# Optimization experiments

Measured on AMD Instinct MI355X. Metric: run time of the kernel, lower is better.

## Reference

```python
import jax, jax.numpy as jnp
import numpy as np
import math

IN_CH = 256; ORDER = 8; K = 9; B = 32; L = 8192


def _conv1d(x, w, b, dilation, padding):
    # x: [B,C,L], w: [O,C,k]
    y = jax.lax.conv_general_dilated(x, w, (1,), [(padding, padding)],
                                     rhs_dilation=(dilation,),
                                     dimension_numbers=('NCH', 'OIH', 'NCH'))
    return y + b[None, :, None]


def _bn(x, g, beta, eps=1e-5):
    # training-mode BatchNorm1d: batch statistics over (B, L), biased variance
    m = x.mean(axis=(0, 2), keepdims=True)
    v = ((x - m) ** 2).mean(axis=(0, 2), keepdims=True)
    return g[None, :, None] * (x - m) * jax.lax.rsqrt(v + eps) + beta[None, :, None]


def _adaptive_r(x, p):
    # p = (c1w,c1b,c2w,c2b,g1,b1,g2,b2,g3,b3,pxw,pxb,fcw,fcb)
    a = jax.nn.relu(_bn(_conv1d(x, p[0], p[1], 1, 1), p[4], p[5]))
    b2 = jax.nn.relu(_bn(_conv1d(x, p[2], p[3], 2, 2), p[6], p[7]))
    c = jax.nn.relu(_bn(_conv1d(a + b2, p[10], p[11], 1, 0), p[8], p[9]))
    pooled = c.mean(axis=2)                      # AdaptiveAvgPool1d(1) + flatten
    return pooled @ p[12].T + p[13]              # [B,1]


def _hermite_kernel(t):
    # t: [B,K] -> kernel [B, ORDER, K]
    hs = [jnp.ones_like(t), 2.0 * t]
    for i in range(2, ORDER - 1):
        hs.append(2.0 * t * hs[-1] - 2.0 * (i - 1) * hs[-2])
    exp_term = jnp.exp(-0.5 * t * t)
    fs = []
    for i in range(ORDER - 1):
        const = 2.0 ** (i / 2) / math.sqrt(math.pi * math.factorial(i))
        f = exp_term * (const * hs[i])
        norm = jnp.linalg.norm(f, axis=1, keepdims=True)
        fs.append(f / jnp.clip(norm, 1e-12))
    fs.append(jax.nn.sigmoid(2.0 * t))           # 1/(1+exp(-2t))
    return jnp.stack(fs, axis=1)


def _forward(x, conv1_w, conv1_b, conv2_b, wp, cp):
    # conv1 is kernel-size-1 -> pointwise GEMM
    x1 = jnp.einsum('bil,oi->bol', x, conv1_w[:, :, 0]) + conv1_b[None, :, None]
    width = _adaptive_r(x1, wp)                  # [B,1]
    center = jnp.clip(_adaptive_r(x1, cp), 1.0, 128.0)
    T = jnp.arange(K, dtype=x.dtype)[None, :]
    t = width * (T - center)                     # [B,K]
    kernel = _hermite_kernel(t)                  # [B,ORDER,K]
    # batched per-sample conv1d (the torch loop over B) as one einsum pass
    pad = K // 2
    Lx = x1.shape[2]
    x1p = jnp.pad(x1, ((0, 0), (0, 0), (pad, pad)))
    out = sum(jnp.einsum('bcl,bc->bl', x1p[:, :, j:j + Lx], kernel[:, :, j])
              for j in range(K))
    out = out[:, None, :] + conv2_b[None, :, None]   # [B,1,L]
    return out, x1


def setup_inputs() -> dict:
    key = jax.random.key(0)
    ks = iter(jax.random.split(key, 64))
    def rn(shape, s=0.05):
        return jax.random.normal(next(ks), shape, dtype=jnp.float32) * s
    d = {
        'x': jax.random.normal(next(ks), (B, IN_CH, L), dtype=jnp.float32),
        'conv1_w': rn((ORDER, IN_CH, 1)),
        'conv1_b': jnp.zeros((ORDER,), jnp.float32),
        'conv2_b': jnp.zeros((1,), jnp.float32),
    }
    for pre in ('w_', 'c_'):
        d[pre + 'c1w'] = rn((ORDER, ORDER, 3)); d[pre + 'c1b'] = jnp.zeros((ORDER,), jnp.float32)
        d[pre + 'c2w'] = rn((ORDER, ORDER, 3)); d[pre + 'c2b'] = jnp.zeros((ORDER,), jnp.float32)
        for g in ('g1', 'g2', 'g3'):
            d[pre + g] = jnp.ones((ORDER,), jnp.float32)
        for bn in ('b1', 'b2', 'b3'):
            d[pre + bn] = jnp.zeros((ORDER,), jnp.float32)
        d[pre + 'pxw'] = rn((ORDER, ORDER, 1)); d[pre + 'pxb'] = jnp.zeros((ORDER,), jnp.float32)
        d[pre + 'fcw'] = rn((1, ORDER), 0.1); d[pre + 'fcb'] = jnp.zeros((1,), jnp.float32)
    return d


def reference(x, conv1_w, conv1_b, conv2_b,
              w_c1w, w_c1b, w_c2w, w_c2b, w_g1, w_b1, w_g2, w_b2, w_g3, w_b3,
              w_pxw, w_pxb, w_fcw, w_fcb,
              c_c1w, c_c1b, c_c2w, c_c2b, c_g1, c_b1, c_g2, c_b2, c_g3, c_b3,
              c_pxw, c_pxb, c_fcw, c_fcb):
    wp = (w_c1w, w_c1b, w_c2w, w_c2b, w_g1, w_b1, w_g2, w_b2, w_g3, w_b3,
          w_pxw, w_pxb, w_fcw, w_fcb)
    cp = (c_c1w, c_c1b, c_c2w, c_c2b, c_g1, c_b1, c_g2, c_b2, c_g3, c_b3,
          c_pxw, c_pxb, c_fcw, c_fcb)
    return _forward(x, conv1_w, conv1_b, conv2_b, wp, cp)
```

## Files before the change

### kernel.cpp

```cpp
#include <hip/hip_runtime.h>
#include <math.h>

#define BATCH 32
#define CIN   256
#define LEN   8192
#define HL    (LEN/2)
#define ORD   8
#define NPOS  (BATCH*LEN)

struct Params { const float* p[32]; };



__device__ __forceinline__ void load_conv_lds(const Params& P, float* wl, float* bl, int tid)
{
    for (int idx = tid; idx < 4*192; idx += 256) {
        int which = idx / 192, s = idx - which*192;
        const float* src = (which==0) ? P.p[4] : (which==1) ? P.p[6]
                         : (which==2) ? P.p[18] : P.p[20];
        wl[idx] = src[s];
    }
    if (tid < 32) {
        int wq = tid >> 3, o = tid & 7;
        const float* bsrc = (wq==0) ? P.p[5] : (wq==1) ? P.p[7]
                          : (wq==2) ? P.p[19] : P.p[21];
        bl[tid] = bsrc[o];
    }
}

__device__ __forceinline__ float conv6(
    const float xv[8][6], const float* wl, const float* bl, int bc, int o, int s)
{
    float a = bl[bc*8 + o];
    const float* wr = &wl[(bc*8 + o)*24];
    if ((bc & 1) == 0) {
#pragma unroll
        for (int i = 0; i < 8; i++)
            a += wr[i*3+0]*xv[i][s+1] + wr[i*3+1]*xv[i][s+2] + wr[i*3+2]*xv[i][s+3];
    } else {
#pragma unroll
        for (int i = 0; i < 8; i++)
            a += wr[i*3+0]*xv[i][s+0] + wr[i*3+1]*xv[i][s+2] + wr[i*3+2]*xv[i][s+4];
    }
    return a;
}

__device__ __forceinline__ void wave_reduce2(float& sv, float& sq)
{
#pragma unroll
    for (int m = 32; m >= 1; m >>= 1) {
        sv += __shfl_xor(sv, m, 64);
        sq += __shfl_xor(sq, m, 64);
    }
}
__device__ __forceinline__ void wave_reduce1(float& sv)
{
#pragma unroll
    for (int m = 32; m >= 1; m >>= 1) sv += __shfl_xor(sv, m, 64);
}

#define XT_W 520
#define LOAD_XV6(xt, tid, xv)                                 \
    _Pragma("unroll")                                         \
    for (int i_ = 0; i_ < 8; i_++) {                          \
        _Pragma("unroll")                                     \
        for (int d_ = 0; d_ < 6; d_++)                        \
            xv[i_][d_] = xt[i_][2 + 2*(tid) + d_];            \
    }

__device__ __forceinline__ void stage_tile(
    const float* __restrict__ x1, int b, int t0, float (*xt)[XT_W], int tid)
{
    int ch = tid >> 5, q = tid & 31;
    const float* src = x1 + ((size_t)b*ORD + ch)*LEN + t0 + q*16;
    float4* dst = reinterpret_cast<float4*>(&xt[ch][4 + q*16]);
#pragma unroll
    for (int j = 0; j < 4; j++) dst[j] = reinterpret_cast<const float4*>(src)[j];
    if (tid < 32) {
        int hc = tid >> 2, hh = tid & 3;
        int l   = t0 + ((hh < 2) ? (hh - 2) : (510 + hh));
        int idx = (hh < 2) ? (2 + hh) : (514 + hh);
        xt[hc][idx] = ((unsigned)l < (unsigned)LEN)
                    ? x1[((size_t)b*ORD + hc)*LEN + l] : 0.f;
    }
}

__global__ __launch_bounds__(256, 2) void k1_gemm_stats(
    const float* __restrict__ x, const float* __restrict__ w,
    const float* __restrict__ bias, float* __restrict__ x1,
    float* __restrict__ ws, Params P)
{
    __shared__ float wt[CIN][ORD];
    __shared__ float wl[768], bl[32];
    __shared__ float xt[8][XT_W];
    __shared__ float part[256];
    int tid = threadIdx.x;
    for (int idx = tid; idx < CIN*ORD; idx += 256) {
        int o = idx >> 8, i = idx & 255;
        wt[i][o] = w[idx];
    }
    load_conv_lds(P, wl, bl, tid);
    __syncthreads();

    int b  = blockIdx.x >> 4;
    int t0 = (blockIdx.x & 15) << 9;

    const float2* xrow = reinterpret_cast<const float2*>(x)
                       + (size_t)b*CIN*HL + (t0 >> 1) + tid;
    float2 acc[ORD];
#pragma unroll
    for (int o = 0; o < ORD; o++) { acc[o].x = 0.f; acc[o].y = 0.f; }

#pragma unroll 8
    for (int i = 0; i < CIN; i++) {
        float2 xv2 = xrow[(size_t)i * HL];
        const float4* wr = reinterpret_cast<const float4*>(&wt[i][0]);
        float4 wa = wr[0], wb = wr[1];
        acc[0].x += xv2.x*wa.x; acc[0].y += xv2.y*wa.x;
        acc[1].x += xv2.x*wa.y; acc[1].y += xv2.y*wa.y;
        acc[2].x += xv2.x*wa.z; acc[2].y += xv2.y*wa.z;
        acc[3].x += xv2.x*wa.w; acc[3].y += xv2.y*wa.w;
        acc[4].x += xv2.x*wb.x; acc[4].y += xv2.y*wb.x;
        acc[5].x += xv2.x*wb.y; acc[5].y += xv2.y*wb.y;
        acc[6].x += xv2.x*wb.z; acc[6].y += xv2.y*wb.z;
        acc[7].x += xv2.x*wb.w; acc[7].y += xv2.y*wb.w;
    }

    float2* x1row = reinterpret_cast<float2*>(x1)
                  + (size_t)b*ORD*HL + (t0 >> 1) + tid;
#pragma unroll
    for (int o = 0; o < ORD; o++) {
        float bo = bias[o];
        float2 r; r.x = acc[o].x + bo; r.y = acc[o].y + bo;
        x1row[(size_t)o * HL] = r;
        *reinterpret_cast<float2*>(&xt[o][4 + 2*tid]) = r;
    }

    if (tid < 32) {
        int hp = tid >> 3, ch = tid & 7;
        int l  = t0 + ((hp < 2) ? (hp - 2) : (510 + hp));
        float a = 0.f;
        if ((unsigned)l < (unsigned)LEN) {
            const float* xp = x + (size_t)b*CIN*LEN + l;
#pragma unroll 4
            for (int i = 0; i < CIN; i++) a += xp[(size_t)i*LEN] * wt[i][ch];
            a += bias[ch];
        }
        int idx = (hp < 2) ? (2 + hp) : (514 + hp);
        xt[ch][idx] = a;
    }
    __syncthreads();

    float xv[8][6];
    LOAD_XV6(xt, tid, xv);

    int lane = tid & 63, wv = tid >> 6;
#pragma unroll
    for (int bc = 0; bc < 4; bc++) {
#pragma unroll
        for (int o = 0; o < 8; o++) {
            float a0 = conv6(xv, wl, bl, bc, o, 0);
            float a1 = conv6(xv, wl, bl, bc, o, 1);
            float sv = a0 + a1, sq = a0*a0 + a1*a1;
            wave_reduce2(sv, sq);
            if (lane == 0) {
                int c = bc*8 + o;
                part[c*4 + wv] = sv; part[(32+c)*4 + wv] = sq;
            }
        }
    }
    __syncthreads();
    if (tid < 64) {
        float s = part[tid*4] + part[tid*4+1] + part[tid*4+2] + part[tid*4+3];
        atomicAdd(&ws[tid], s);
    }
}

__global__ __launch_bounds__(256, 2) void k3_cpre_stats(
    const float* __restrict__ x1, float* __restrict__ ws, Params P)
{
    __shared__ float wl[768], bl[32];
    __shared__ float pxl[128], pxbl[16];
    __shared__ float scl[32], shf[32];
    __shared__ float xt[8][XT_W];
    __shared__ float part[128];
    int tid = threadIdx.x;
    load_conv_lds(P, wl, bl, tid);
    if (tid < 128) pxl[tid]  = (tid < 64) ? P.p[14][tid] : P.p[28][tid-64];
    if (tid < 16)  pxbl[tid] = (tid < 8)  ? P.p[15][tid] : P.p[29][tid-8];
    if (tid >= 128 && tid < 160) {
        int c = tid - 128;
        int br = c >> 4, cv = (c >> 3) & 1, o = c & 7;
        const float Ninv = 1.0f / (float)NPOS;
        float m   = ws[c]      * Ninv;
        float var = ws[32 + c] * Ninv - m*m;
        const float* g  = P.p[ br ? (cv?23:22) : (cv?9:8)  ];
        const float* be = P.p[ br ? (cv?26:25) : (cv?12:11)];
        float sc = g[o] * rsqrtf(var + 1e-5f);
        scl[c] = sc; shf[c] = be[o] - m*sc;
    }
    int b  = blockIdx.x >> 4;
    int t0 = (blockIdx.x & 15) << 9;
    stage_tile(x1, b, t0, xt, tid);
    __syncthreads();

    float xv[8][6];
    LOAD_XV6(xt, tid, xv);

    int lane = tid & 63, wv = tid >> 6;
#pragma unroll
    for (int br = 0; br < 2; br++) {
        float s0[8], s1[8];
#pragma unroll
        for (int ch = 0; ch < 8; ch++) {
            int ca = (br*2+0)*8 + ch, cb = (br*2+1)*8 + ch;
            s0[ch] = fmaxf(conv6(xv,wl,bl,br*2+0,ch,0)*scl[ca] + shf[ca], 0.f)
                   + fmaxf(conv6(xv,wl,bl,br*2+1,ch,0)*scl[cb] + shf[cb], 0.f);
            s1[ch] = fmaxf(conv6(xv,wl,bl,br*2+0,ch,1)*scl[ca] + shf[ca], 0.f)
                   + fmaxf(conv6(xv,wl,bl,br*2+1,ch,1)*scl[cb] + shf[cb], 0.f);
        }
#pragma unroll
        for (int o = 0; o < 8; o++) {
            float a0 = pxbl[br*8 + o], a1 = a0;
#pragma unroll
            for (int i = 0; i < 8; i++) {
                a0 += pxl[br*64 + o*8 + i] * s0[i];
                a1 += pxl[br*64 + o*8 + i] * s1[i];
            }
            float sv = a0 + a1, sq = a0*a0 + a1*a1;
            wave_reduce2(sv, sq);
            if (lane == 0) {
                int c = br*8 + o;
                part[c*4 + wv] = sv; part[(16+c)*4 + wv] = sq;
            }
        }
    }
    __syncthreads();
    if (tid < 32) {
        float s = part[tid*4] + part[tid*4+1] + part[tid*4+2] + part[tid*4+3];
        atomicAdd(&ws[64 + tid], s);
    }
}

__global__ __launch_bounds__(256, 2) void k4_csum(
    const float* __restrict__ x1, float* __restrict__ ws, Params P)
{
    __shared__ float wl[768], bl[32];
    __shared__ float pxl[128], pxbl[16];
    __shared__ float scl[32], shf[32];
    __shared__ float scl3[16], shf3[16];
    __shared__ float xt[8][XT_W];
    __shared__ float part[64];
    int tid = threadIdx.x;
    load_conv_lds(P, wl, bl, tid);
    if (tid < 128) pxl[tid]  = (tid < 64) ? P.p[14][tid] : P.p[28][tid-64];
    if (tid < 16)  pxbl[tid] = (tid < 8)  ? P.p[15][tid] : P.p[29][tid-8];
    const float Ninv = 1.0f / (float)NPOS;
    if (tid >= 128 && tid < 160) {
        int c = tid - 128;
        int br = c >> 4, cv = (c >> 3) & 1, o = c & 7;
        float m   = ws[c]      * Ninv;
        float var = ws[32 + c] * Ninv - m*m;
        const float* g  = P.p[ br ? (cv?23:22) : (cv?9:8)  ];
        const float* be = P.p[ br ? (cv?26:25) : (cv?12:11)];
        float sc = g[o] * rsqrtf(var + 1e-5f);
        scl[c] = sc; shf[c] = be[o] - m*sc;
    }
    if (tid >= 160 && tid < 176) {
        int c = tid - 160;
        int br = c >> 3, o = c & 7;
        float m3 = ws[64 + c] * Ninv;
        float v3 = ws[80 + c] * Ninv - m3*m3;
        const float* g3 = P.p[ br ? 24 : 10 ];
        const float* b3 = P.p[ br ? 27 : 13 ];
        float sc = g3[o] * rsqrtf(v3 + 1e-5f);
        scl3[c] = sc; shf3[c] = b3[o] - m3*sc;
    }
    int b  = blockIdx.x >> 4;
    int t0 = (blockIdx.x & 15) << 9;
    stage_tile(x1, b, t0, xt, tid);
    __syncthreads();

    float xv[8][6];
    LOAD_XV6(xt, tid, xv);

    int lane = tid & 63, wv = tid >> 6;
#pragma unroll
    for (int br = 0; br < 2; br++) {
        float s0[8], s1[8];
#pragma unroll
        for (int ch = 0; ch < 8; ch++) {
            int ca = (br*2+0)*8 + ch, cb = (br*2+1)*8 + ch;
            s0[ch] = fmaxf(conv6(xv,wl,bl,br*2+0,ch,0)*scl[ca] + shf[ca], 0.f)
                   + fmaxf(conv6(xv,wl,bl,br*2+1,ch,0)*scl[cb] + shf[cb], 0.f);
            s1[ch] = fmaxf(conv6(xv,wl,bl,br*2+0,ch,1)*scl[ca] + shf[ca], 0.f)
                   + fmaxf(conv6(xv,wl,bl,br*2+1,ch,1)*scl[cb] + shf[cb], 0.f);
        }
#pragma unroll
        for (int o = 0; o < 8; o++) {
            float a0 = pxbl[br*8 + o], a1 = a0;
#pragma unroll
            for (int i = 0; i < 8; i++) {
                a0 += pxl[br*64 + o*8 + i] * s0[i];
                a1 += pxl[br*64 + o*8 + i] * s1[i];
            }
            int c = br*8 + o;
            float v0 = fmaxf(a0*scl3[c] + shf3[c], 0.f);
            float v1 = fmaxf(a1*scl3[c] + shf3[c], 0.f);
            float sv = v0 + v1;
            wave_reduce1(sv);
            if (lane == 0) part[c*4 + wv] = sv;
        }
    }
    __syncthreads();
    if (tid < 16) {
        float s = part[tid*4] + part[tid*4+1] + part[tid*4+2] + part[tid*4+3];
        atomicAdd(&ws[96 + (tid >> 3)*256 + b*8 + (tid & 7)], s);
    }
}

#define XT6_W 272
__global__ __launch_bounds__(256) void k6_out(
    const float* __restrict__ x1, const float* __restrict__ ws, Params P,
    float* __restrict__ out)
{
    __shared__ float kern[8][9];
    __shared__ float xt[8][XT6_W];
    int tid = threadIdx.x;
    int b  = blockIdx.x >> 5;
    int t0 = (blockIdx.x & 31) << 8;

    {
        int ch = tid >> 5, q = tid & 31;
        const float* src = x1 + ((size_t)b*ORD + ch)*LEN + t0;
        float4 a0 = *reinterpret_cast<const float4*>(src + q*8);
        float4 a1 = *reinterpret_cast<const float4*>(src + q*8 + 4);
        *reinterpret_cast<float4*>(&xt[ch][8  + q*8]) = a0;
        *reinterpret_cast<float4*>(&xt[ch][12 + q*8]) = a1;
        if (q < 4) {
            int l = t0 - 4 + q;
            xt[ch][4 + q] = (l >= 0) ? src[q - 4] : 0.f;
        } else if (q < 8) {
            int l = t0 + 256 + (q - 4);
            xt[ch][260 + q] = (l < LEN) ? src[256 + q - 4] : 0.f;
        }
    }

    if (tid < 9) {
        const float Li = 1.0f / (float)LEN;
        float vw = P.p[17][0], vc = P.p[31][0];
#pragma unroll
        for (int ch = 0; ch < 8; ch++) {
            vw += P.p[16][ch] * (ws[96 +       b*8 + ch] * Li);
            vc += P.p[30][ch] * (ws[96 + 256 + b*8 + ch] * Li);
        }
        float width  = vw;
        float center = fminf(fmaxf(vc, 1.0f), 128.0f);

        float cst[7];
        cst[0] = 0.56418958354775628f;
#pragma unroll
        for (int i = 1; i < 7; i++) cst[i] = cst[i-1] * sqrtf(2.0f / (float)i);

        int k = tid;
        float t = width * ((float)k - center);
        float e = expf(-0.5f * t * t);
        float hp = 1.0f, hc = 2.0f * t;
        kern[0][k] = e * cst[0];
        kern[1][k] = e * cst[1] * hc;
#pragma unroll
        for (int i = 2; i < 7; i++) {
            float hn = 2.0f*t*hc - 2.0f*(float)(i-1)*hp;
            hp = hc; hc = hn;
            kern[i][k] = e * cst[i] * hc;
        }
        kern[7][k] = 1.0f / (1.0f + expf(-2.0f * t));
    }
    __syncthreads();
    if (tid < 7) {
        float ss = 0.f;
#pragma unroll
        for (int k = 0; k < 9; k++) ss += kern[tid][k]*kern[tid][k];
        float inv = 1.0f / fmaxf(sqrtf(ss), 1e-12f);
#pragma unroll
        for (int k = 0; k < 9; k++) kern[tid][k] *= inv;
    }
    __syncthreads();

    float acc = P.p[3][0];
#pragma unroll
    for (int c = 0; c < 8; c++) {
#pragma unroll
        for (int j = 0; j < 9; j++) acc += xt[c][4 + tid + j] * kern[c][j];
    }
    out[(size_t)b*LEN + t0 + tid] = acc;
}

extern "C" void kernel_launch(void* const* d_in, const int* in_sizes, int n_in,
                              void* d_out, int out_size, void* d_ws, size_t ws_size,
                              hipStream_t stream)
{
    (void)in_sizes; (void)n_in; (void)out_size; (void)ws_size;
    const float* x  = (const float*)d_in[0];
    const float* w1 = (const float*)d_in[1];
    const float* b1 = (const float*)d_in[2];
    float* outF = (float*)d_out;
    float* x1   = outF + (size_t)BATCH * LEN;
    float* ws   = (float*)d_ws;

    Params P;
    for (int i = 0; i < 32; i++) P.p[i] = (const float*)d_in[i];

    hipMemsetAsync(d_ws, 0, 4096, stream);
    k1_gemm_stats<<<512,  256, 0, stream>>>(x, w1, b1, x1, ws, P);
    k3_cpre_stats<<<512,  256, 0, stream>>>(x1, ws, P);
    k4_csum      <<<512,  256, 0, stream>>>(x1, ws, P);
    k6_out       <<<1024, 256, 0, stream>>>(x1, ws, P, outF);
}
```

Baseline: 142.6 us.

## Materialize pre-BN3 activations to skip recomputing convs in csum pass

The third stats pass no longer recomputes the dilated convolutions and pointwise mix. It now reads 16 pre-BN channels that the second pass writes to workspace, which trades compute for an extra write and read of about 32 MB. The GEMM kernel also loads its halo inputs with a coalesced per-channel load into LDS instead of strided global reads. Conv weights are now read directly through restrict pointers rather than staged in LDS. The workspace must be large enough to hold cpre.

```diff
diff --git a/kernel.cpp b/kernel.cpp
--- a/kernel.cpp
+++ b/kernel.cpp
@@ -12,37 +12,24 @@
 
 
 
-__device__ __forceinline__ void load_conv_lds(const Params& P, float* wl, float* bl, int tid)
-{
-    for (int idx = tid; idx < 4*192; idx += 256) {
-        int which = idx / 192, s = idx - which*192;
-        const float* src = (which==0) ? P.p[4] : (which==1) ? P.p[6]
-                         : (which==2) ? P.p[18] : P.p[20];
-        wl[idx] = src[s];
-    }
-    if (tid < 32) {
-        int wq = tid >> 3, o = tid & 7;
-        const float* bsrc = (wq==0) ? P.p[5] : (wq==1) ? P.p[7]
-                          : (wq==2) ? P.p[19] : P.p[21];
-        bl[tid] = bsrc[o];
-    }
-}
-
-__device__ __forceinline__ float conv6(
-    const float xv[8][6], const float* wl, const float* bl, int bc, int o, int s)
-{
-    float a = bl[bc*8 + o];
-    const float* wr = &wl[(bc*8 + o)*24];
-    if ((bc & 1) == 0) {
-#pragma unroll
-        for (int i = 0; i < 8; i++)
-            a += wr[i*3+0]*xv[i][s+1] + wr[i*3+1]*xv[i][s+2] + wr[i*3+2]*xv[i][s+3];
-    } else {
-#pragma unroll
-        for (int i = 0; i < 8; i++)
-            a += wr[i*3+0]*xv[i][s+0] + wr[i*3+1]*xv[i][s+2] + wr[i*3+2]*xv[i][s+4];
-    }
-    return a;
+__device__ __forceinline__ void conv6_pair(
+    const float xv[8][6], const float* __restrict__ w, float bv, int dil, int o,
+    float& r0, float& r1)
+{
+    float a0 = bv, a1 = bv;
+    const float* wr = w + o*24;
+#pragma unroll
+    for (int i = 0; i < 8; i++) {
+        float w0 = wr[i*3+0], w1 = wr[i*3+1], w2 = wr[i*3+2];
+        if (dil == 1) {
+            a0 += w0*xv[i][1] + w1*xv[i][2] + w2*xv[i][3];
+            a1 += w0*xv[i][2] + w1*xv[i][3] + w2*xv[i][4];
+        } else {
+            a0 += w0*xv[i][0] + w1*xv[i][2] + w2*xv[i][4];
+            a1 += w0*xv[i][1] + w1*xv[i][3] + w2*xv[i][5];
+        }
+    }
+    r0 = a0; r1 = a1;
 }
 
 __device__ __forceinline__ void wave_reduce2(float& sv, float& sq)
@@ -88,22 +75,30 @@
 __global__ __launch_bounds__(256, 2) void k1_gemm_stats(
     const float* __restrict__ x, const float* __restrict__ w,
     const float* __restrict__ bias, float* __restrict__ x1,
-    float* __restrict__ ws, Params P)
+    float* __restrict__ ws,
+    const float* __restrict__ wA, const float* __restrict__ bA,
+    const float* __restrict__ wB, const float* __restrict__ bB,
+    const float* __restrict__ wC, const float* __restrict__ bC,
+    const float* __restrict__ wD, const float* __restrict__ bD)
 {
     __shared__ float wt[CIN][ORD];
-    __shared__ float wl[768], bl[32];
     __shared__ float xt[8][XT_W];
+    __shared__ float hbuf[4][257];
     __shared__ float part[256];
     int tid = threadIdx.x;
     for (int idx = tid; idx < CIN*ORD; idx += 256) {
         int o = idx >> 8, i = idx & 255;
         wt[i][o] = w[idx];
     }
-    load_conv_lds(P, wl, bl, tid);
-    __syncthreads();
 
     int b  = blockIdx.x >> 4;
     int t0 = (blockIdx.x & 15) << 9;
+
+    const float* xch = x + ((size_t)b*CIN + tid)*LEN;
+    float h0 = 0.f, h1 = 0.f, h2 = 0.f, h3 = 0.f;
+    if (t0 >= 2)        { h0 = xch[t0-2];   h1 = xch[t0-1]; }
+    if (t0 + 513 < LEN) { h2 = xch[t0+512]; h3 = xch[t0+513]; }
+    __syncthreads();
 
     const float2* xrow = reinterpret_cast<const float2*>(x)
                        + (size_t)b*CIN*HL + (t0 >> 1) + tid;
@@ -135,16 +130,17 @@
         x1row[(size_t)o * HL] = r;
         *reinterpret_cast<float2*>(&xt[o][4 + 2*tid]) = r;
     }
+    hbuf[0][tid] = h0; hbuf[1][tid] = h1; hbuf[2][tid] = h2; hbuf[3][tid] = h3;
+    __syncthreads();
 
     if (tid < 32) {
         int hp = tid >> 3, ch = tid & 7;
         int l  = t0 + ((hp < 2) ? (hp - 2) : (510 + hp));
         float a = 0.f;
         if ((unsigned)l < (unsigned)LEN) {
-            const float* xp = x + (size_t)b*CIN*LEN + l;
-#pragma unroll 4
-            for (int i = 0; i < CIN; i++) a += xp[(size_t)i*LEN] * wt[i][ch];
-            a += bias[ch];
+            a = bias[ch];
+#pragma unroll 8
+            for (int i = 0; i < CIN; i++) a += hbuf[hp][i] * wt[i][ch];
         }
         int idx = (hp < 2) ? (2 + hp) : (514 + hp);
         xt[ch][idx] = a;
@@ -156,15 +152,18 @@
 
     int lane = tid & 63, wv = tid >> 6;
 #pragma unroll
-    for (int bc = 0; bc < 4; bc++) {
+    for (int grp = 0; grp < 4; grp++) {
+        const float* wg = (grp==0) ? wA : (grp==1) ? wB : (grp==2) ? wC : wD;
+        const float* bg = (grp==0) ? bA : (grp==1) ? bB : (grp==2) ? bC : bD;
+        int dil = (grp & 1) ? 2 : 1;
 #pragma unroll
         for (int o = 0; o < 8; o++) {
-            float a0 = conv6(xv, wl, bl, bc, o, 0);
-            float a1 = conv6(xv, wl, bl, bc, o, 1);
+            float a0, a1;
+            conv6_pair(xv, wg, bg[o], dil, o, a0, a1);
             float sv = a0 + a1, sq = a0*a0 + a1*a1;
             wave_reduce2(sv, sq);
             if (lane == 0) {
-                int c = bc*8 + o;
+                int c = grp*8 + o;
                 part[c*4 + wv] = sv; part[(32+c)*4 + wv] = sq;
             }
         }
@@ -177,17 +176,19 @@
 }
 
 __global__ __launch_bounds__(256, 2) void k3_cpre_stats(
-    const float* __restrict__ x1, float* __restrict__ ws, Params P)
-{
-    __shared__ float wl[768], bl[32];
-    __shared__ float pxl[128], pxbl[16];
+    const float* __restrict__ x1,
+    const float* __restrict__ wA, const float* __restrict__ bA,
+    const float* __restrict__ wB, const float* __restrict__ bB,
+    const float* __restrict__ wC, const float* __restrict__ bC,
+    const float* __restrict__ wD, const float* __restrict__ bD,
+    const float* __restrict__ pxA, const float* __restrict__ pxbA,
+    const float* __restrict__ pxB, const float* __restrict__ pxbB,
+    float* __restrict__ ws, float* __restrict__ cpre, Params P)
+{
     __shared__ float scl[32], shf[32];
     __shared__ float xt[8][XT_W];
     __shared__ float part[128];
     int tid = threadIdx.x;
-    load_conv_lds(P, wl, bl, tid);
-    if (tid < 128) pxl[tid]  = (tid < 64) ? P.p[14][tid] : P.p[28][tid-64];
-    if (tid < 16)  pxbl[tid] = (tid < 8)  ? P.p[15][tid] : P.p[29][tid-8];
     if (tid >= 128 && tid < 160) {
         int c = tid - 128;
         int br = c >> 4, cv = (c >> 3) & 1, o = c & 7;
@@ -210,27 +211,37 @@
     int lane = tid & 63, wv = tid >> 6;
 #pragma unroll
     for (int br = 0; br < 2; br++) {
+        const float* w1p = br ? wC : wA;  const float* b1p = br ? bC : bA;
+        const float* w2p = br ? wD : wB;  const float* b2p = br ? bD : bB;
+        const float* pxp = br ? pxB : pxA;
+        const float* pbp = br ? pxbB : pxbA;
         float s0[8], s1[8];
 #pragma unroll
         for (int ch = 0; ch < 8; ch++) {
             int ca = (br*2+0)*8 + ch, cb = (br*2+1)*8 + ch;
-            s0[ch] = fmaxf(conv6(xv,wl,bl,br*2+0,ch,0)*scl[ca] + shf[ca], 0.f)
-                   + fmaxf(conv6(xv,wl,bl,br*2+1,ch,0)*scl[cb] + shf[cb], 0.f);
-            s1[ch] = fmaxf(conv6(xv,wl,bl,br*2+0,ch,1)*scl[ca] + shf[ca], 0.f)
-                   + fmaxf(conv6(xv,wl,bl,br*2+1,ch,1)*scl[cb] + shf[cb], 0.f);
+            float a0, a1, c0, c1;
+            conv6_pair(xv, w1p, b1p[ch], 1, ch, a0, a1);
+            conv6_pair(xv, w2p, b2p[ch], 2, ch, c0, c1);
+            s0[ch] = fmaxf(a0*scl[ca] + shf[ca], 0.f)
+                   + fmaxf(c0*scl[cb] + shf[cb], 0.f);
+            s1[ch] = fmaxf(a1*scl[ca] + shf[ca], 0.f)
+                   + fmaxf(c1*scl[cb] + shf[cb], 0.f);
         }
 #pragma unroll
         for (int o = 0; o < 8; o++) {
-            float a0 = pxbl[br*8 + o], a1 = a0;
+            float a0 = pbp[o], a1 = a0;
 #pragma unroll
             for (int i = 0; i < 8; i++) {
-                a0 += pxl[br*64 + o*8 + i] * s0[i];
-                a1 += pxl[br*64 + o*8 + i] * s1[i];
+                a0 += pxp[o*8 + i] * s0[i];
+                a1 += pxp[o*8 + i] * s1[i];
             }
+            int c = br*8 + o;
+            float2 st; st.x = a0; st.y = a1;
+            *reinterpret_cast<float2*>(
+                &cpre[(size_t)c*NPOS + (size_t)b*LEN + t0 + 2*tid]) = st;
             float sv = a0 + a1, sq = a0*a0 + a1*a1;
             wave_reduce2(sv, sq);
             if (lane == 0) {
-                int c = br*8 + o;
                 part[c*4 + wv] = sv; part[(16+c)*4 + wv] = sq;
             }
         }
@@ -242,75 +253,35 @@
     }
 }
 
-__global__ __launch_bounds__(256, 2) void k4_csum(
-    const float* __restrict__ x1, float* __restrict__ ws, Params P)
-{
-    __shared__ float wl[768], bl[32];
-    __shared__ float pxl[128], pxbl[16];
-    __shared__ float scl[32], shf[32];
+__global__ __launch_bounds__(256) void k4_light(
+    const float* __restrict__ cpre, float* __restrict__ ws, Params P)
+{
     __shared__ float scl3[16], shf3[16];
-    __shared__ float xt[8][XT_W];
     __shared__ float part[64];
     int tid = threadIdx.x;
-    load_conv_lds(P, wl, bl, tid);
-    if (tid < 128) pxl[tid]  = (tid < 64) ? P.p[14][tid] : P.p[28][tid-64];
-    if (tid < 16)  pxbl[tid] = (tid < 8)  ? P.p[15][tid] : P.p[29][tid-8];
     const float Ninv = 1.0f / (float)NPOS;
-    if (tid >= 128 && tid < 160) {
-        int c = tid - 128;
-        int br = c >> 4, cv = (c >> 3) & 1, o = c & 7;
-        float m   = ws[c]      * Ninv;
-        float var = ws[32 + c] * Ninv - m*m;
-        const float* g  = P.p[ br ? (cv?23:22) : (cv?9:8)  ];
-        const float* be = P.p[ br ? (cv?26:25) : (cv?12:11)];
-        float sc = g[o] * rsqrtf(var + 1e-5f);
-        scl[c] = sc; shf[c] = be[o] - m*sc;
-    }
-    if (tid >= 160 && tid < 176) {
-        int c = tid - 160;
-        int br = c >> 3, o = c & 7;
-        float m3 = ws[64 + c] * Ninv;
-        float v3 = ws[80 + c] * Ninv - m3*m3;
+    if (tid < 16) {
+        int br = tid >> 3, o = tid & 7;
+        float m3 = ws[64 + tid] * Ninv;
+        float v3 = ws[80 + tid] * Ninv - m3*m3;
         const float* g3 = P.p[ br ? 24 : 10 ];
         const float* b3 = P.p[ br ? 27 : 13 ];
         float sc = g3[o] * rsqrtf(v3 + 1e-5f);
-        scl3[c] = sc; shf3[c] = b3[o] - m3*sc;
-    }
+        scl3[tid] = sc; shf3[tid] = b3[o] - m3*sc;
+    }
+    __syncthreads();
+
     int b  = blockIdx.x >> 4;
     int t0 = (blockIdx.x & 15) << 9;
-    stage_tile(x1, b, t0, xt, tid);
-    __syncthreads();
-
-    float xv[8][6];
-    LOAD_XV6(xt, tid, xv);
-
     int lane = tid & 63, wv = tid >> 6;
 #pragma unroll
-    for (int br = 0; br < 2; br++) {
-        float s0[8], s1[8];
-#pragma unroll
-        for (int ch = 0; ch < 8; ch++) {
-            int ca = (br*2+0)*8 + ch, cb = (br*2+1)*8 + ch;
-            s0[ch] = fmaxf(conv6(xv,wl,bl,br*2+0,ch,0)*scl[ca] + shf[ca], 0.f)
-                   + fmaxf(conv6(xv,wl,bl,br*2+1,ch,0)*scl[cb] + shf[cb], 0.f);
-            s1[ch] = fmaxf(conv6(xv,wl,bl,br*2+0,ch,1)*scl[ca] + shf[ca], 0.f)
-                   + fmaxf(conv6(xv,wl,bl,br*2+1,ch,1)*scl[cb] + shf[cb], 0.f);
-        }
-#pragma unroll
-        for (int o = 0; o < 8; o++) {
-            float a0 = pxbl[br*8 + o], a1 = a0;
-#pragma unroll
-            for (int i = 0; i < 8; i++) {
-                a0 += pxl[br*64 + o*8 + i] * s0[i];
-                a1 += pxl[br*64 + o*8 + i] * s1[i];
-            }
-            int c = br*8 + o;
-            float v0 = fmaxf(a0*scl3[c] + shf3[c], 0.f);
-            float v1 = fmaxf(a1*scl3[c] + shf3[c], 0.f);
-            float sv = v0 + v1;
-            wave_reduce1(sv);
-            if (lane == 0) part[c*4 + wv] = sv;
-        }
+    for (int c = 0; c < 16; c++) {
+        float2 v = *reinterpret_cast<const float2*>(
+            &cpre[(size_t)c*NPOS + (size_t)b*LEN + t0 + 2*tid]);
+        float sv = fmaxf(v.x*scl3[c] + shf3[c], 0.f)
+                 + fmaxf(v.y*scl3[c] + shf3[c], 0.f);
+        wave_reduce1(sv);
+        if (lane == 0) part[c*4 + wv] = sv;
     }
     __syncthreads();
     if (tid < 16) {
@@ -407,13 +378,22 @@
     float* outF = (float*)d_out;
     float* x1   = outF + (size_t)BATCH * LEN;
     float* ws   = (float*)d_ws;
+    float* cpre = ws + 1024;
 
     Params P;
     for (int i = 0; i < 32; i++) P.p[i] = (const float*)d_in[i];
 
+    const float* wA = P.p[4],  *bA = P.p[5];
+    const float* wB = P.p[6],  *bB = P.p[7];
+    const float* wC = P.p[18], *bC = P.p[19];
+    const float* wD = P.p[20], *bD = P.p[21];
+
     hipMemsetAsync(d_ws, 0, 4096, stream);
-    k1_gemm_stats<<<512,  256, 0, stream>>>(x, w1, b1, x1, ws, P);
-    k3_cpre_stats<<<512,  256, 0, stream>>>(x1, ws, P);
-    k4_csum      <<<512,  256, 0, stream>>>(x1, ws, P);
+    k1_gemm_stats<<<512,  256, 0, stream>>>(x, w1, b1, x1, ws,
+                                            wA, bA, wB, bB, wC, bC, wD, bD);
+    k3_cpre_stats<<<512,  256, 0, stream>>>(x1, wA, bA, wB, bB, wC, bC, wD, bD,
+                                            P.p[14], P.p[15], P.p[28], P.p[29],
+                                            ws, cpre, P);
+    k4_light     <<<512,  256, 0, stream>>>(cpre, ws, P);
     k6_out       <<<1024, 256, 0, stream>>>(x1, ws, P, outF);
 }
```

Result: faster. 133.5 us (-6.4%).

## Fuse pooling and output conv via last-block-per-batch pattern; cache halo inputs

Applied to the files above, without the earlier changes.

The separate pooling and output-convolution kernels are merged into one. The last block to finish each batch, found with an atomic counter, builds the Hermite kernel and computes the whole 8192-length output row in 1024-wide chunks, which removes one launch. In the GEMM kernel, each thread loads the halo x values for its channel up front into LDS, replacing the strided global-memory dot products done by 32 threads. The conv weight loads are also vectorised through float4 reads into registers. The trade-off is that the final output stage now runs on only 32 blocks, one per batch, which serialises that work and may leave most of the GPU idle.

```diff
diff --git a/kernel.cpp b/kernel.cpp
--- a/kernel.cpp
+++ b/kernel.cpp
@@ -11,6 +11,19 @@
 struct Params { const float* p[32]; };
 
 
+__device__ __forceinline__ void wave_reduce2(float& sv, float& sq)
+{
+#pragma unroll
+    for (int m = 32; m >= 1; m >>= 1) {
+        sv += __shfl_xor(sv, m, 64);
+        sq += __shfl_xor(sq, m, 64);
+    }
+}
+__device__ __forceinline__ void wave_reduce1(float& sv)
+{
+#pragma unroll
+    for (int m = 32; m >= 1; m >>= 1) sv += __shfl_xor(sv, m, 64);
+}
 
 __device__ __forceinline__ void load_conv_lds(const Params& P, float* wl, float* bl, int tid)
 {
@@ -28,48 +41,32 @@
     }
 }
 
-__device__ __forceinline__ float conv6(
-    const float xv[8][6], const float* wl, const float* bl, int bc, int o, int s)
-{
-    float a = bl[bc*8 + o];
-    const float* wr = &wl[(bc*8 + o)*24];
-    if ((bc & 1) == 0) {
-#pragma unroll
-        for (int i = 0; i < 8; i++)
-            a += wr[i*3+0]*xv[i][s+1] + wr[i*3+1]*xv[i][s+2] + wr[i*3+2]*xv[i][s+3];
-    } else {
-#pragma unroll
-        for (int i = 0; i < 8; i++)
-            a += wr[i*3+0]*xv[i][s+0] + wr[i*3+1]*xv[i][s+2] + wr[i*3+2]*xv[i][s+4];
-    }
-    return a;
-}
-
-__device__ __forceinline__ void wave_reduce2(float& sv, float& sq)
-{
-#pragma unroll
-    for (int m = 32; m >= 1; m >>= 1) {
-        sv += __shfl_xor(sv, m, 64);
-        sq += __shfl_xor(sq, m, 64);
-    }
-}
-__device__ __forceinline__ void wave_reduce1(float& sv)
-{
-#pragma unroll
-    for (int m = 32; m >= 1; m >>= 1) sv += __shfl_xor(sv, m, 64);
-}
-
-#define XT_W 520
-#define LOAD_XV6(xt, tid, xv)                                 \
-    _Pragma("unroll")                                         \
-    for (int i_ = 0; i_ < 8; i_++) {                          \
-        _Pragma("unroll")                                     \
-        for (int d_ = 0; d_ < 6; d_++)                        \
-            xv[i_][d_] = xt[i_][2 + 2*(tid) + d_];            \
-    }
-
+__device__ __forceinline__ void conv6_pair_lds(
+    const float xv[8][6], const float* wl, float bv, int dil, int row,
+    float& r0, float& r1)
+{
+    float a0 = bv, a1 = bv;
+    const float4* wr4 = reinterpret_cast<const float4*>(wl + row*24);
+    float wr[24];
+#pragma unroll
+    for (int q = 0; q < 6; q++) *reinterpret_cast<float4*>(&wr[4*q]) = wr4[q];
+#pragma unroll
+    for (int i = 0; i < 8; i++) {
+        float w0 = wr[i*3+0], w1 = wr[i*3+1], w2 = wr[i*3+2];
+        if (dil == 1) {
+            a0 += w0*xv[i][1] + w1*xv[i][2] + w2*xv[i][3];
+            a1 += w0*xv[i][2] + w1*xv[i][3] + w2*xv[i][4];
+        } else {
+            a0 += w0*xv[i][0] + w1*xv[i][2] + w2*xv[i][4];
+            a1 += w0*xv[i][1] + w1*xv[i][3] + w2*xv[i][5];
+        }
+    }
+    r0 = a0; r1 = a1;
+}
+
+template<int W>
 __device__ __forceinline__ void stage_tile(
-    const float* __restrict__ x1, int b, int t0, float (*xt)[XT_W], int tid)
+    const float* __restrict__ x1, int b, int t0, float (*xt)[W], int tid)
 {
     int ch = tid >> 5, q = tid & 31;
     const float* src = x1 + ((size_t)b*ORD + ch)*LEN + t0 + q*16;
@@ -85,14 +82,23 @@
     }
 }
 
+#define LOAD_XV6(xt, tid, xv)                                 \
+    _Pragma("unroll")                                         \
+    for (int i_ = 0; i_ < 8; i_++) {                          \
+        _Pragma("unroll")                                     \
+        for (int d_ = 0; d_ < 6; d_++)                        \
+            xv[i_][d_] = xt[i_][2 + 2*(tid) + d_];            \
+    }
+
 __global__ __launch_bounds__(256, 2) void k1_gemm_stats(
     const float* __restrict__ x, const float* __restrict__ w,
     const float* __restrict__ bias, float* __restrict__ x1,
     float* __restrict__ ws, Params P)
 {
     __shared__ float wt[CIN][ORD];
+    __shared__ float xt[ORD][528];
+    __shared__ float hbuf[4][257];
     __shared__ float wl[768], bl[32];
-    __shared__ float xt[8][XT_W];
     __shared__ float part[256];
     int tid = threadIdx.x;
     for (int idx = tid; idx < CIN*ORD; idx += 256) {
@@ -100,10 +106,15 @@
         wt[i][o] = w[idx];
     }
     load_conv_lds(P, wl, bl, tid);
-    __syncthreads();
 
     int b  = blockIdx.x >> 4;
     int t0 = (blockIdx.x & 15) << 9;
+
+    const float* xch = x + ((size_t)b*CIN + tid)*LEN;
+    float h0 = 0.f, h1 = 0.f, h2 = 0.f, h3 = 0.f;
+    if (t0 >= 2)        { h0 = xch[t0-2];   h1 = xch[t0-1]; }
+    if (t0 + 513 < LEN) { h2 = xch[t0+512]; h3 = xch[t0+513]; }
+    __syncthreads();
 
     const float2* xrow = reinterpret_cast<const float2*>(x)
                        + (size_t)b*CIN*HL + (t0 >> 1) + tid;
@@ -135,18 +146,19 @@
         x1row[(size_t)o * HL] = r;
         *reinterpret_cast<float2*>(&xt[o][4 + 2*tid]) = r;
     }
+    hbuf[0][tid] = h0; hbuf[1][tid] = h1; hbuf[2][tid] = h2; hbuf[3][tid] = h3;
+    __syncthreads();
 
     if (tid < 32) {
-        int hp = tid >> 3, ch = tid & 7;
-        int l  = t0 + ((hp < 2) ? (hp - 2) : (510 + hp));
+        int hq = tid >> 3, ch = tid & 7;
+        int l  = t0 + ((hq < 2) ? (hq - 2) : (510 + hq));
         float a = 0.f;
         if ((unsigned)l < (unsigned)LEN) {
-            const float* xp = x + (size_t)b*CIN*LEN + l;
-#pragma unroll 4
-            for (int i = 0; i < CIN; i++) a += xp[(size_t)i*LEN] * wt[i][ch];
-            a += bias[ch];
-        }
-        int idx = (hp < 2) ? (2 + hp) : (514 + hp);
+            a = bias[ch];
+#pragma unroll 8
+            for (int i = 0; i < CIN; i++) a += hbuf[hq][i] * wt[i][ch];
+        }
+        int idx = (hq < 2) ? (2 + hq) : (514 + hq);
         xt[ch][idx] = a;
     }
     __syncthreads();
@@ -156,17 +168,16 @@
 
     int lane = tid & 63, wv = tid >> 6;
 #pragma unroll
-    for (int bc = 0; bc < 4; bc++) {
+    for (int grp = 0; grp < 4; grp++) {
+        int dil = (grp & 1) ? 2 : 1;
 #pragma unroll
         for (int o = 0; o < 8; o++) {
-            float a0 = conv6(xv, wl, bl, bc, o, 0);
-            float a1 = conv6(xv, wl, bl, bc, o, 1);
+            int c = grp*8 + o;
+            float a0, a1;
+            conv6_pair_lds(xv, wl, bl[c], dil, c, a0, a1);
             float sv = a0 + a1, sq = a0*a0 + a1*a1;
             wave_reduce2(sv, sq);
-            if (lane == 0) {
-                int c = bc*8 + o;
-                part[c*4 + wv] = sv; part[(32+c)*4 + wv] = sq;
-            }
+            if (lane == 0) { part[c*4 + wv] = sv; part[(32+c)*4 + wv] = sq; }
         }
     }
     __syncthreads();
@@ -176,20 +187,20 @@
     }
 }
 
-__global__ __launch_bounds__(256, 2) void k3_cpre_stats(
+__global__ __launch_bounds__(256, 2) void k3_stats(
     const float* __restrict__ x1, float* __restrict__ ws, Params P)
 {
     __shared__ float wl[768], bl[32];
     __shared__ float pxl[128], pxbl[16];
     __shared__ float scl[32], shf[32];
-    __shared__ float xt[8][XT_W];
+    __shared__ float xt[ORD][528];
     __shared__ float part[128];
     int tid = threadIdx.x;
     load_conv_lds(P, wl, bl, tid);
-    if (tid < 128) pxl[tid]  = (tid < 64) ? P.p[14][tid] : P.p[28][tid-64];
-    if (tid < 16)  pxbl[tid] = (tid < 8)  ? P.p[15][tid] : P.p[29][tid-8];
-    if (tid >= 128 && tid < 160) {
-        int c = tid - 128;
+    if (tid >= 128) { int q = tid - 128; pxl[q] = (q < 64) ? P.p[14][q] : P.p[28][q-64]; }
+    if (tid >= 112 && tid < 128) { int q = tid - 112; pxbl[q] = (q < 8) ? P.p[15][q] : P.p[29][q-8]; }
+    if (tid >= 32 && tid < 64) {
+        int c = tid - 32;
         int br = c >> 4, cv = (c >> 3) & 1, o = c & 7;
         const float Ninv = 1.0f / (float)NPOS;
         float m   = ws[c]      * Ninv;
@@ -201,7 +212,7 @@
     }
     int b  = blockIdx.x >> 4;
     int t0 = (blockIdx.x & 15) << 9;
-    stage_tile(x1, b, t0, xt, tid);
+    stage_tile<528>(x1, b, t0, xt, tid);
     __syncthreads();
 
     float xv[8][6];
@@ -214,10 +225,11 @@
 #pragma unroll
         for (int ch = 0; ch < 8; ch++) {
             int ca = (br*2+0)*8 + ch, cb = (br*2+1)*8 + ch;
-            s0[ch] = fmaxf(conv6(xv,wl,bl,br*2+0,ch,0)*scl[ca] + shf[ca], 0.f)
-                   + fmaxf(conv6(xv,wl,bl,br*2+1,ch,0)*scl[cb] + shf[cb], 0.f);
-            s1[ch] = fmaxf(conv6(xv,wl,bl,br*2+0,ch,1)*scl[ca] + shf[ca], 0.f)
-                   + fmaxf(conv6(xv,wl,bl,br*2+1,ch,1)*scl[cb] + shf[cb], 0.f);
+            float a0, a1, c0, c1;
+            conv6_pair_lds(xv, wl, bl[ca], 1, ca, a0, a1);
+            conv6_pair_lds(xv, wl, bl[cb], 2, cb, c0, c1);
+            s0[ch] = fmaxf(a0*scl[ca] + shf[ca], 0.f) + fmaxf(c0*scl[cb] + shf[cb], 0.f);
+            s1[ch] = fmaxf(a1*scl[ca] + shf[ca], 0.f) + fmaxf(c1*scl[cb] + shf[cb], 0.f);
         }
 #pragma unroll
         for (int o = 0; o < 8; o++) {
@@ -227,12 +239,10 @@
                 a0 += pxl[br*64 + o*8 + i] * s0[i];
                 a1 += pxl[br*64 + o*8 + i] * s1[i];
             }
+            int c = br*8 + o;
             float sv = a0 + a1, sq = a0*a0 + a1*a1;
             wave_reduce2(sv, sq);
-            if (lane == 0) {
-                int c = br*8 + o;
-                part[c*4 + wv] = sv; part[(16+c)*4 + wv] = sq;
-            }
+            if (lane == 0) { part[c*4 + wv] = sv; part[(16+c)*4 + wv] = sq; }
         }
     }
     __syncthreads();
@@ -242,22 +252,25 @@
     }
 }
 
-__global__ __launch_bounds__(256, 2) void k4_csum(
-    const float* __restrict__ x1, float* __restrict__ ws, Params P)
+#define SROW 1040
+__global__ __launch_bounds__(256, 2) void k46_pool_out(
+    const float* __restrict__ x1, float* __restrict__ ws, Params P,
+    float* __restrict__ out)
 {
     __shared__ float wl[768], bl[32];
     __shared__ float pxl[128], pxbl[16];
-    __shared__ float scl[32], shf[32];
-    __shared__ float scl3[16], shf3[16];
-    __shared__ float xt[8][XT_W];
+    __shared__ float scl[32], shf[32], scl3[16], shf3[16];
+    __shared__ float smem[ORD][SROW];
     __shared__ float part[64];
+    __shared__ float kern[8][9];
+    __shared__ int amLast;
     int tid = threadIdx.x;
+    const float Ninv = 1.0f / (float)NPOS;
     load_conv_lds(P, wl, bl, tid);
-    if (tid < 128) pxl[tid]  = (tid < 64) ? P.p[14][tid] : P.p[28][tid-64];
-    if (tid < 16)  pxbl[tid] = (tid < 8)  ? P.p[15][tid] : P.p[29][tid-8];
-    const float Ninv = 1.0f / (float)NPOS;
-    if (tid >= 128 && tid < 160) {
-        int c = tid - 128;
+    if (tid >= 128) { int q = tid - 128; pxl[q] = (q < 64) ? P.p[14][q] : P.p[28][q-64]; }
+    if (tid >= 112 && tid < 128) { int q = tid - 112; pxbl[q] = (q < 8) ? P.p[15][q] : P.p[29][q-8]; }
+    if (tid >= 32 && tid < 64) {
+        int c = tid - 32;
         int br = c >> 4, cv = (c >> 3) & 1, o = c & 7;
         float m   = ws[c]      * Ninv;
         float var = ws[32 + c] * Ninv - m*m;
@@ -266,8 +279,8 @@
         float sc = g[o] * rsqrtf(var + 1e-5f);
         scl[c] = sc; shf[c] = be[o] - m*sc;
     }
-    if (tid >= 160 && tid < 176) {
-        int c = tid - 160;
+    if (tid >= 64 && tid < 80) {
+        int c = tid - 64;
         int br = c >> 3, o = c & 7;
         float m3 = ws[64 + c] * Ninv;
         float v3 = ws[80 + c] * Ninv - m3*m3;
@@ -278,11 +291,11 @@
     }
     int b  = blockIdx.x >> 4;
     int t0 = (blockIdx.x & 15) << 9;
-    stage_tile(x1, b, t0, xt, tid);
+    stage_tile<SROW>(x1, b, t0, smem, tid);
     __syncthreads();
 
     float xv[8][6];
-    LOAD_XV6(xt, tid, xv);
+    LOAD_XV6(smem, tid, xv);
 
     int lane = tid & 63, wv = tid >> 6;
 #pragma unroll
@@ -291,10 +304,11 @@
 #pragma unroll
         for (int ch = 0; ch < 8; ch++) {
             int ca = (br*2+0)*8 + ch, cb = (br*2+1)*8 + ch;
-            s0[ch] = fmaxf(conv6(xv,wl,bl,br*2+0,ch,0)*scl[ca] + shf[ca], 0.f)
-                   + fmaxf(conv6(xv,wl,bl,br*2+1,ch,0)*scl[cb] + shf[cb], 0.f);
-            s1[ch] = fmaxf(conv6(xv,wl,bl,br*2+0,ch,1)*scl[ca] + shf[ca], 0.f)
-                   + fmaxf(conv6(xv,wl,bl,br*2+1,ch,1)*scl[cb] + shf[cb], 0.f);
+            float a0, a1, c0, c1;
+            conv6_pair_lds(xv, wl, bl[ca], 1, ca, a0, a1);
+            conv6_pair_lds(xv, wl, bl[cb], 2, cb, c0, c1);
+            s0[ch] = fmaxf(a0*scl[ca] + shf[ca], 0.f) + fmaxf(c0*scl[cb] + shf[cb], 0.f);
+            s1[ch] = fmaxf(a1*scl[ca] + shf[ca], 0.f) + fmaxf(c1*scl[cb] + shf[cb], 0.f);
         }
 #pragma unroll
         for (int o = 0; o < 8; o++) {
@@ -305,9 +319,8 @@
                 a1 += pxl[br*64 + o*8 + i] * s1[i];
             }
             int c = br*8 + o;
-            float v0 = fmaxf(a0*scl3[c] + shf3[c], 0.f);
-            float v1 = fmaxf(a1*scl3[c] + shf3[c], 0.f);
-            float sv = v0 + v1;
+            float sv = fmaxf(a0*scl3[c] + shf3[c], 0.f)
+                     + fmaxf(a1*scl3[c] + shf3[c], 0.f);
             wave_reduce1(sv);
             if (lane == 0) part[c*4 + wv] = sv;
         }
@@ -317,61 +330,42 @@
         float s = part[tid*4] + part[tid*4+1] + part[tid*4+2] + part[tid*4+3];
         atomicAdd(&ws[96 + (tid >> 3)*256 + b*8 + (tid & 7)], s);
     }
-}
-
-#define XT6_W 272
-__global__ __launch_bounds__(256) void k6_out(
-    const float* __restrict__ x1, const float* __restrict__ ws, Params P,
-    float* __restrict__ out)
-{
-    __shared__ float kern[8][9];
-    __shared__ float xt[8][XT6_W];
-    int tid = threadIdx.x;
-    int b  = blockIdx.x >> 5;
-    int t0 = (blockIdx.x & 31) << 8;
-
-    {
-        int ch = tid >> 5, q = tid & 31;
-        const float* src = x1 + ((size_t)b*ORD + ch)*LEN + t0;
-        float4 a0 = *reinterpret_cast<const float4*>(src + q*8);
-        float4 a1 = *reinterpret_cast<const float4*>(src + q*8 + 4);
-        *reinterpret_cast<float4*>(&xt[ch][8  + q*8]) = a0;
-        *reinterpret_cast<float4*>(&xt[ch][12 + q*8]) = a1;
-        if (q < 4) {
-            int l = t0 - 4 + q;
-            xt[ch][4 + q] = (l >= 0) ? src[q - 4] : 0.f;
-        } else if (q < 8) {
-            int l = t0 + 256 + (q - 4);
-            xt[ch][260 + q] = (l < LEN) ? src[256 + q - 4] : 0.f;
-        }
-    }
+    __threadfence();
+    __syncthreads();
+    if (tid == 0) {
+        int* cnt = (int*)(ws + 608);
+        int old = atomicAdd(&cnt[b], 1);
+        amLast = (old == 15);
+    }
+    __syncthreads();
+    if (!amLast) return;
+    __threadfence();
 
     if (tid < 9) {
+        const volatile float* wsp = ws;
         const float Li = 1.0f / (float)LEN;
         float vw = P.p[17][0], vc = P.p[31][0];
 #pragma unroll
         for (int ch = 0; ch < 8; ch++) {
-            vw += P.p[16][ch] * (ws[96 +       b*8 + ch] * Li);
-            vc += P.p[30][ch] * (ws[96 + 256 + b*8 + ch] * Li);
+            vw += P.p[16][ch] * (wsp[96 +       b*8 + ch] * Li);
+            vc += P.p[30][ch] * (wsp[96 + 256 + b*8 + ch] * Li);
         }
         float width  = vw;
         float center = fminf(fmaxf(vc, 1.0f), 128.0f);
-
         float cst[7];
         cst[0] = 0.56418958354775628f;
 #pragma unroll
         for (int i = 1; i < 7; i++) cst[i] = cst[i-1] * sqrtf(2.0f / (float)i);
-
         int k = tid;
         float t = width * ((float)k - center);
         float e = expf(-0.5f * t * t);
-        float hp = 1.0f, hc = 2.0f * t;
+        float hpv = 1.0f, hc = 2.0f * t;
         kern[0][k] = e * cst[0];
         kern[1][k] = e * cst[1] * hc;
 #pragma unroll
         for (int i = 2; i < 7; i++) {
-            float hn = 2.0f*t*hc - 2.0f*(float)(i-1)*hp;
-            hp = hc; hc = hn;
+            float hn = 2.0f*t*hc - 2.0f*(float)(i-1)*hpv;
+            hpv = hc; hc = hn;
             kern[i][k] = e * cst[i] * hc;
         }
         kern[7][k] = 1.0f / (1.0f + expf(-2.0f * t));
@@ -385,15 +379,41 @@
 #pragma unroll
         for (int k = 0; k < 9; k++) kern[tid][k] *= inv;
     }
-    __syncthreads();
-
-    float acc = P.p[3][0];
-#pragma unroll
-    for (int c = 0; c < 8; c++) {
-#pragma unroll
-        for (int j = 0; j < 9; j++) acc += xt[c][4 + tid + j] * kern[c][j];
-    }
-    out[(size_t)b*LEN + t0 + tid] = acc;
+
+    const float c2b = P.p[3][0];
+    float* outp = out + (size_t)b*LEN;
+    for (int ck = 0; ck < 8; ck++) {
+        __syncthreads();
+        {
+            int ch = tid >> 5, q = tid & 31;
+            const float* src = x1 + ((size_t)b*ORD + ch)*LEN + ck*1024;
+            float4* dst = reinterpret_cast<float4*>(&smem[ch][4]);
+#pragma unroll
+            for (int r = 0; r < 8; r++) {
+                int f4 = q + 32*r;
+                dst[f4] = reinterpret_cast<const float4*>(src)[f4];
+            }
+            if (tid < 64) {
+                int hc = tid >> 3, hh = tid & 7;
+                int l, idx;
+                if (hh < 4) { l = ck*1024 - 4 + hh;        idx = hh; }
+                else        { l = ck*1024 + 1024 + (hh-4); idx = 1028 + (hh-4); }
+                smem[hc][idx] = ((unsigned)l < (unsigned)LEN)
+                              ? x1[((size_t)b*ORD + hc)*LEN + l] : 0.f;
+            }
+        }
+        __syncthreads();
+#pragma unroll
+        for (int q2 = 0; q2 < 4; q2++) {
+            int p = tid + 256*q2;
+            float a = c2b;
+#pragma unroll
+            for (int c = 0; c < 8; c++)
+#pragma unroll
+                for (int j = 0; j < 9; j++) a += smem[c][p + j] * kern[c][j];
+            outp[ck*1024 + p] = a;
+        }
+    }
 }
 
 extern "C" void kernel_launch(void* const* d_in, const int* in_sizes, int n_in,
@@ -412,8 +432,7 @@
     for (int i = 0; i < 32; i++) P.p[i] = (const float*)d_in[i];
 
     hipMemsetAsync(d_ws, 0, 4096, stream);
-    k1_gemm_stats<<<512,  256, 0, stream>>>(x, w1, b1, x1, ws, P);
-    k3_cpre_stats<<<512,  256, 0, stream>>>(x1, ws, P);
-    k4_csum      <<<512,  256, 0, stream>>>(x1, ws, P);
-    k6_out       <<<1024, 256, 0, stream>>>(x1, ws, P, outF);
-}
+    k1_gemm_stats<<<512, 256, 0, stream>>>(x, w1, b1, x1, ws, P);
+    k3_stats     <<<512, 256, 0, stream>>>(x1, ws, P);
+    k46_pool_out <<<512, 256, 0, stream>>>(x1, ws, P, outF);
+}
```

New measurement: 191.7 us. 1.34x slower.
